# Optimization experiments

Hardware: AMD Instinct MI355X
Metric: run time of the kernel (lower is better)

The kernel has to match this reference:

```python
import jax, jax.numpy as jnp
import numpy as np
from jax.scipy.special import logsumexp

_INF = 1e8
_GAMMA_MIN = 1e-4


def _cosine_cost(x, y):
    # 1 - cosine similarity, batched: [B,M,D] x [B,N,D] -> [B,M,N]
    xn = x / jnp.clip(jnp.linalg.norm(x, axis=-1, keepdims=True), 1e-8)
    yn = y / jnp.clip(jnp.linalg.norm(y, axis=-1, keepdims=True), 1e-8)
    return 1.0 - jnp.einsum('bmd,bnd->bmn', xn, yn)


def _soft_dtw_alignment(cost, gv):
    B, M, N = cost.shape
    dt = cost.dtype
    ii = jnp.arange(M)          # full diagonal index range, masked per step

    # ---- forward DP: R[b, i+1, j+1] = C[i,j] + softmin(R[i,j], R[i,j+1], R[i+1,j]) ----
    R0 = jnp.full((B, M + 1, N + 1), _INF, dtype=dt).at[:, 0, 0].set(0.0)

    def fstep(R, d):
        jj = d - ii
        valid = (jj >= 0) & (jj < N)            # (M,)
        jjc = jnp.clip(jj, 0, N - 1)
        ip, jp = ii + 1, jjc + 1
        p = jnp.stack([R[:, ip - 1, jp - 1],
                       R[:, ip - 1, jp],
                       R[:, ip, jp - 1]], axis=-1)          # (B, M, 3)
        soft = -gv * logsumexp(p / -gv, axis=-1)            # soft-min
        new = cost[:, ii, jjc] + soft                       # (B, M)
        cur = R[:, ip, jp]
        R = R.at[:, ip, jp].set(jnp.where(valid[None, :], new, cur))
        return R, None

    R, _ = jax.lax.scan(fstep, R0, jnp.arange(M + N - 1))
    distance = R[:, M, N]

    # ---- backward DP for alignment matrix E ----
    E0 = jnp.zeros((B, M + 2, N + 2), dtype=dt).at[:, M, N].set(1.0)
    Re = jnp.full((B, M + 2, N + 2), -_INF, dtype=dt).at[:, :M + 1, :N + 1].set(R)
    Ce = jnp.zeros((B, M + 2, N + 2), dtype=dt).at[:, 1:M + 1, 1:N + 1].set(cost)

    def bstep(E, d):
        jj = d - ii
        valid = (jj >= 0) & (jj < N)
        jjc = jnp.clip(jj, 0, N - 1)
        ip, jp = ii + 1, jjc + 1
        rc = Re[:, ip, jp]
        wd = jnp.exp(jnp.clip((Re[:, ip + 1, jp + 1] - Ce[:, ip + 1, jp + 1] - rc) / gv, -50, 50))
        wn = jnp.exp(jnp.clip((Re[:, ip + 1, jp] - Ce[:, ip + 1, jp] - rc) / gv, -50, 50))
        wr = jnp.exp(jnp.clip((Re[:, ip, jp + 1] - Ce[:, ip, jp + 1] - rc) / gv, -50, 50))
        new = E[:, ip + 1, jp + 1] * wd + E[:, ip + 1, jp] * wn + E[:, ip, jp + 1] * wr
        cur = E[:, ip, jp]
        E = E.at[:, ip, jp].set(jnp.where(valid[None, :], new, cur))
        return E, None

    E, _ = jax.lax.scan(bstep, E0, jnp.arange(M + N - 3, -1, -1))
    alignment = E[:, 1:M + 1, 1:N + 1]
    return alignment, distance


def setup_inputs() -> dict:
    key = jax.random.key(0)
    k1, k2 = jax.random.split(key)
    B, M, N, D = 8, 256, 256, 512
    x = jax.random.normal(k1, (B, M, D), dtype=jnp.float32)
    y = jax.random.normal(k2, (B, N, D), dtype=jnp.float32)
    gamma = jnp.asarray(1.0, dtype=jnp.float32)   # learned nn.Parameter
    return {"x": x, "y": y, "gamma": gamma}


def reference(x, y, gamma):
    cost = _cosine_cost(x, y)
    gv = jnp.maximum(jnp.abs(gamma), _GAMMA_MIN)   # effective gamma
    alignment, distance = _soft_dtw_alignment(cost, gv)
    return alignment, distance
```

## Files before the change

### kernel.cpp

```cpp
#include <hip/hip_runtime.h>

#define USTR 192

#define EXP2F(x) __builtin_amdgcn_exp2f(x)
#define LOG2F(x) __builtin_amdgcn_logf(x)

__device__ __forceinline__ void ld4(float d[4], const float* p) {
  float4 v = *(const float4*)p;
  d[0] = v.x; d[1] = v.y; d[2] = v.z; d[3] = v.w;
}

__global__ void __launch_bounds__(256) norms_kernel(const float* __restrict__ x,
                                                    const float* __restrict__ y,
                                                    float* __restrict__ rnx,
                                                    float* __restrict__ rny) {
  int g = blockIdx.x * 4 + (threadIdx.x >> 6);
  int lane = threadIdx.x & 63;
  const float* src; float* dst; int row;
  if (g < 2048) { src = x; dst = rnx; row = g; }
  else          { src = y; dst = rny; row = g - 2048; }
  const float* p = src + (size_t)row * 512;
  float4 v0 = *(const float4*)(p + lane * 4);
  float4 v1 = *(const float4*)(p + 256 + lane * 4);
  float s = v0.x*v0.x + v0.y*v0.y + v0.z*v0.z + v0.w*v0.w
          + v1.x*v1.x + v1.y*v1.y + v1.z*v1.z + v1.w*v1.w;
#pragma unroll
  for (int o = 32; o > 0; o >>= 1) s += __shfl_xor(s, o, 64);
  if (lane == 0) dst[row] = 1.0f / fmaxf(sqrtf(s), 1e-8f);
}

__global__ void __launch_bounds__(256) cost_gemm(const float* __restrict__ x,
                                                 const float* __restrict__ y,
                                                 const float* __restrict__ rnx,
                                                 const float* __restrict__ rny,
                                                 const float* __restrict__ gamma,
                                                 float* __restrict__ mAll) {
  int b = blockIdx.z, mt = blockIdx.y, nt = blockIdx.x;
  int m0 = mt * 32, n0 = nt * 64;
  __shared__ float Xs[16][36];
  __shared__ float Ys[16][68];
  int tid = threadIdx.x;
  int row = tid >> 2, cq = tid & 3;
  int tx = tid & 15, ty = tid >> 4;
  const float* xb = x + ((size_t)b * 256 + m0) * 512;
  const float* yb = y + ((size_t)b * 256 + n0) * 512;
  float acc[2][4] = {};
  for (int k0 = 0; k0 < 512; k0 += 16) {
    float4 xv;
    if (tid < 128) xv = *(const float4*)(xb + (size_t)row * 512 + k0 + cq * 4);
    float4 yv = *(const float4*)(yb + (size_t)row * 512 + k0 + cq * 4);
    __syncthreads();
    if (tid < 128) {
      Xs[cq*4+0][row] = xv.x; Xs[cq*4+1][row] = xv.y;
      Xs[cq*4+2][row] = xv.z; Xs[cq*4+3][row] = xv.w;
    }
    Ys[cq*4+0][row] = yv.x; Ys[cq*4+1][row] = yv.y;
    Ys[cq*4+2][row] = yv.z; Ys[cq*4+3][row] = yv.w;
    __syncthreads();
#pragma unroll
    for (int kk = 0; kk < 16; ++kk) {
      float a0 = Xs[kk][ty * 2 + 0];
      float a1 = Xs[kk][ty * 2 + 1];
      float4 bv = *(const float4*)(&Ys[kk][tx * 4]);
      float br[4] = {bv.x, bv.y, bv.z, bv.w};
#pragma unroll
      for (int c = 0; c < 4; ++c) {
        acc[0][c] += a0 * br[c];
        acc[1][c] += a1 * br[c];
      }
    }
  }
  float gv = fmaxf(fabsf(gamma[0]), 1e-4f);
  float ig2 = 1.4426950408889634f / gv;
  float rx[2], ry[4];
#pragma unroll
  for (int r = 0; r < 2; ++r) rx[r] = rnx[b * 256 + m0 + ty * 2 + r];
#pragma unroll
  for (int c = 0; c < 4; ++c) ry[c] = rny[b * 256 + n0 + tx * 4 + c];
  int l = nt * 16 + tx;
  int v = mt * 16 + ty;
  int u = v + l;
  float4 stm[2];
#pragma unroll
  for (int r = 0; r < 2; ++r) {
    float c0 = (1.0f - acc[r][0] * rx[r] * ry[0]) * ig2;
    float c1 = (1.0f - acc[r][1] * rx[r] * ry[1]) * ig2;
    float c2 = (1.0f - acc[r][2] * rx[r] * ry[2]) * ig2;
    float c3 = (1.0f - acc[r][3] * rx[r] * ry[3]) * ig2;
    stm[r] = (float4){EXP2F(-c0), EXP2F(-c1), EXP2F(-c2), EXP2F(-c3)};
  }
  float* mpF = mAll + ((size_t)b * USTR + u) * 512 + l * 8;
  *(float4*)(mpF)     = stm[0];
  *(float4*)(mpF + 4) = stm[1];
  float* mpR = mAll + ((size_t)(8 + b) * USTR + (190 - u)) * 512 + (63 - l) * 8;
  *(float4*)(mpR)     = (float4){stm[1].w, stm[1].z, stm[1].y, stm[1].x};
  *(float4*)(mpR + 4) = (float4){stm[0].w, stm[0].z, stm[0].y, stm[0].x};
}

__global__ void __launch_bounds__(64, 1) pass_kernel(const float* __restrict__ mAll,
                                                     float* __restrict__ pAll,
                                                     float* __restrict__ QepAll,
                                                     const float* __restrict__ gamma,
                                                     float* __restrict__ dist_out) {
  int blk = blockIdx.x, l = threadIdx.x;
  int dir = blk >> 3, b = blk & 7;
  float gv = fmaxf(fabsf(gamma[0]), 1e-4f);
  float gl = gv * 0.6931471805599453f;
  const float* mb = mAll + (size_t)blk * USTR * 512 + l * 8;
  float* pb = pAll + (size_t)blk * USTR * 512 + l * 8;
  float* qe = QepAll + ((size_t)blk * 64 + l) * 24;
  float Pp0 = 0.f, Pp1 = 0.f, Pp2 = 0.f, Pp3 = 0.f;
  float bot0 = 0.f, bot1 = 0.f;
  int Q = 0;
  float ucar = (l == 0) ? 1.0f : 0.f;
  float A0[8], A1[8], A2[8], A3[8], A4[8], A5[8], A6[8], A7[8];
  float A8[8], A9[8], A10[8], A11[8], A12[8], A13[8], A14[8], A15[8];
  auto loadC = [&](int t, float* buf) {
    int u = t > 190 ? 190 : t;
    const float* p = mb + (size_t)u * 512;
    ld4(buf, p); ld4(buf + 4, p + 4);
  };
  auto body = [&](int t, const float* mm) {
    bool act = (unsigned)(t - l) <= 127u;
    float s0 = __shfl_up(bot0, 1);
    float s1 = __shfl_up(bot1, 1);
    int  liQ = __shfl_up(Q, 1);
    if (l == 0) { s0 = 0.f; s1 = 0.f; }
    else { int adj = liQ - Q; s0 = ldexpf(s0, adj); s1 = ldexpf(s1, adj); }
    float v0 = mm[0] * (Pp0 + s0 + ucar);
    float v1 = mm[1] * (Pp1 + v0 + Pp0);
    float v2 = mm[2] * (Pp2 + v1 + Pp1);
    float v3 = mm[3] * (Pp3 + v2 + Pp2);
    float w0 = mm[4] * (v0 + s1 + s0);
    float w1 = mm[5] * (v1 + w0 + v0);
    float w2 = mm[6] * (v2 + w1 + v1);
    float w3 = mm[7] * (v3 + w2 + v2);
    if (act) {
      float* sp = pb + (size_t)t * 512;
      *(float4*)(sp)     = (float4){v0, v1, v2, v3};
      *(float4*)(sp + 4) = (float4){w0, w1, w2, w3};
      Pp0 = w0; Pp1 = w1; Pp2 = w2; Pp3 = w3;
      ucar = s1; bot0 = v3; bot1 = w3;
      if (dir == 0 && l == 63 && t == 190)
        dist_out[b] = (-(float)Q - LOG2F(w3)) * gl;
    }
  };
  auto renorm = [&](int tEnd) {
    if ((unsigned)(tEnd - l) <= 127u) {
      int e = (int)((__float_as_uint(Pp3) >> 23) & 255u) - 127;
      Pp0 = ldexpf(Pp0, -e); Pp1 = ldexpf(Pp1, -e);
      Pp2 = ldexpf(Pp2, -e); Pp3 = ldexpf(Pp3, -e);
      ucar = ldexpf(ucar, -e);
      bot0 = ldexpf(bot0, -e); bot1 = ldexpf(bot1, -e);
      Q += e;
    }
  };
  loadC(0, A0);  loadC(1, A1);  loadC(2, A2);  loadC(3, A3);
  loadC(4, A4);  loadC(5, A5);  loadC(6, A6);  loadC(7, A7);
  loadC(8, A8);  loadC(9, A9);  loadC(10, A10); loadC(11, A11);
  loadC(12, A12); loadC(13, A13); loadC(14, A14); loadC(15, A15);
  for (int it = 0; it < 12; ++it) {
    int s = it * 16;
    qe[2 * it] = (float)Q;
    body(s + 0, A0); loadC(s + 16, A0);
    body(s + 1, A1); loadC(s + 17, A1);
    body(s + 2, A2); loadC(s + 18, A2);
    body(s + 3, A3); loadC(s + 19, A3);
    body(s + 4, A4); loadC(s + 20, A4);
    body(s + 5, A5); loadC(s + 21, A5);
    body(s + 6, A6); loadC(s + 22, A6);
    body(s + 7, A7); loadC(s + 23, A7);
    renorm(s + 7);
    qe[2 * it + 1] = (float)Q;
    body(s + 8,  A8);  loadC(s + 24, A8);
    body(s + 9,  A9);  loadC(s + 25, A9);
    body(s + 10, A10); loadC(s + 26, A10);
    body(s + 11, A11); loadC(s + 27, A11);
    body(s + 12, A12); loadC(s + 28, A12);
    body(s + 13, A13); loadC(s + 29, A13);
    body(s + 14, A14); loadC(s + 30, A14);
    body(s + 15, A15); loadC(s + 31, A15);
    renorm(s + 15);
  }
}

__global__ void __launch_bounds__(256) e_kernel(const float* __restrict__ mAll,
                                                const float* __restrict__ pAll,
                                                const float* __restrict__ QepAll,
                                                float* __restrict__ out) {
  int tid = blockIdx.x * 256 + threadIdx.x;
  int l = tid & 63;
  int r = (tid >> 6) & 255;
  int b = tid >> 14;
  int v = r >> 1, rf = r & 1;
  int uF = v + l;
  int uR = 190 - v - l;
  const float* pF  = pAll + ((size_t)b * USTR + uF) * 512 + l * 8 + rf * 4;
  const float* pRv = pAll + ((size_t)(8 + b) * USTR + uR) * 512 + (63 - l) * 8 + (1 - rf) * 4;
  const float* mF  = mAll + ((size_t)b * USTR + uF) * 512 + l * 8 + rf * 4;
  float P[4], Bv[4], M[4];
  ld4(P, pF); ld4(Bv, pRv); ld4(M, mF);
  float Qf = QepAll[((size_t)b * 64 + l) * 24 + (uF >> 3)];
  float Qb = QepAll[((size_t)(8 + b) * 64 + (63 - l)) * 24 + (uR >> 3)];
  float Zp = pAll[((size_t)b * USTR + 190) * 512 + 511];
  float Zq = QepAll[((size_t)b * 64 + 63) * 24 + 23];
  int e = (int)(Qf + Qb - Zq);
  float inv = 1.0f / Zp;
  float4 o;
  o.x = ldexpf(P[0] * Bv[3] / M[0] * inv, e);
  o.y = ldexpf(P[1] * Bv[2] / M[1] * inv, e);
  o.z = ldexpf(P[2] * Bv[1] / M[2] * inv, e);
  o.w = ldexpf(P[3] * Bv[0] / M[3] * inv, e);
  *(float4*)(out + (size_t)b * 65536 + (size_t)r * 256 + 4 * l) = o;
}

extern "C" void kernel_launch(void* const* d_in, const int* in_sizes, int n_in,
                              void* d_out, int out_size, void* d_ws, size_t ws_size,
                              hipStream_t stream) {
  const float* x = (const float*)d_in[0];
  const float* y = (const float*)d_in[1];
  const float* gamma = (const float*)d_in[2];
  float* out = (float*)d_out;
  float* ws = (float*)d_ws;

  const size_t PMAT = (size_t)16 * USTR * 512;
  float* rnx    = ws;
  float* rny    = ws + 2048;
  float* mAll   = ws + 4096;
  float* pAll   = mAll + PMAT;
  float* QepAll = pAll + PMAT;

  norms_kernel<<<1024, 256, 0, stream>>>(x, y, rnx, rny);
  cost_gemm<<<dim3(4, 8, 8), 256, 0, stream>>>(x, y, rnx, rny, gamma, mAll);
  pass_kernel<<<16, 64, 0, stream>>>(mAll, pAll, QepAll, gamma, out + 524288);
  e_kernel<<<512, 256, 0, stream>>>(mAll, pAll, QepAll, out);
}
```

Measured before the change: 125.7 us.

## Fuse row-norm computation into cost GEMM and double-buffer its K tiles

Removes the separate norms kernel: row sums of squares are accumulated from the tiles already loaded by the cost GEMM, reduced with lane shuffles, and kept in shared memory. The GEMM main loop now uses K tiles of 32 with double-buffered shared memory and prefetches the next tile into registers during compute, halving the barriers per K. This saves one launch and a re-read of x and y, at the cost of more registers and shared memory per block.

```diff
diff --git a/kernel.cpp b/kernel.cpp
--- a/kernel.cpp
+++ b/kernel.cpp
@@ -10,58 +10,61 @@
   d[0] = v.x; d[1] = v.y; d[2] = v.z; d[3] = v.w;
 }
 
-__global__ void __launch_bounds__(256) norms_kernel(const float* __restrict__ x,
-                                                    const float* __restrict__ y,
-                                                    float* __restrict__ rnx,
-                                                    float* __restrict__ rny) {
-  int g = blockIdx.x * 4 + (threadIdx.x >> 6);
-  int lane = threadIdx.x & 63;
-  const float* src; float* dst; int row;
-  if (g < 2048) { src = x; dst = rnx; row = g; }
-  else          { src = y; dst = rny; row = g - 2048; }
-  const float* p = src + (size_t)row * 512;
-  float4 v0 = *(const float4*)(p + lane * 4);
-  float4 v1 = *(const float4*)(p + 256 + lane * 4);
-  float s = v0.x*v0.x + v0.y*v0.y + v0.z*v0.z + v0.w*v0.w
-          + v1.x*v1.x + v1.y*v1.y + v1.z*v1.z + v1.w*v1.w;
-#pragma unroll
-  for (int o = 32; o > 0; o >>= 1) s += __shfl_xor(s, o, 64);
-  if (lane == 0) dst[row] = 1.0f / fmaxf(sqrtf(s), 1e-8f);
-}
-
 __global__ void __launch_bounds__(256) cost_gemm(const float* __restrict__ x,
                                                  const float* __restrict__ y,
-                                                 const float* __restrict__ rnx,
-                                                 const float* __restrict__ rny,
                                                  const float* __restrict__ gamma,
                                                  float* __restrict__ mAll) {
   int b = blockIdx.z, mt = blockIdx.y, nt = blockIdx.x;
   int m0 = mt * 32, n0 = nt * 64;
-  __shared__ float Xs[16][36];
-  __shared__ float Ys[16][68];
+  __shared__ float Xs[2][32][36];
+  __shared__ float Ys[2][32][68];
+  __shared__ float RxS[32];
+  __shared__ float RyS[64];
   int tid = threadIdx.x;
   int row = tid >> 2, cq = tid & 3;
   int tx = tid & 15, ty = tid >> 4;
   const float* xb = x + ((size_t)b * 256 + m0) * 512;
   const float* yb = y + ((size_t)b * 256 + n0) * 512;
   float acc[2][4] = {};
-  for (int k0 = 0; k0 < 512; k0 += 16) {
-    float4 xv;
-    if (tid < 128) xv = *(const float4*)(xb + (size_t)row * 512 + k0 + cq * 4);
-    float4 yv = *(const float4*)(yb + (size_t)row * 512 + k0 + cq * 4);
+  float sx = 0.f, sy = 0.f;
+  float4 xv0, xv1, yv0, yv1;
+
+  auto loadTile = [&](int k0) {
+    if (tid < 128) {
+      xv0 = *(const float4*)(xb + (size_t)row * 512 + k0 + cq * 4);
+      xv1 = *(const float4*)(xb + (size_t)row * 512 + k0 + 16 + cq * 4);
+    }
+    yv0 = *(const float4*)(yb + (size_t)row * 512 + k0 + cq * 4);
+    yv1 = *(const float4*)(yb + (size_t)row * 512 + k0 + 16 + cq * 4);
+  };
+  auto stageTile = [&](int buf) {
+    if (tid < 128) {
+      sx += xv0.x*xv0.x + xv0.y*xv0.y + xv0.z*xv0.z + xv0.w*xv0.w
+          + xv1.x*xv1.x + xv1.y*xv1.y + xv1.z*xv1.z + xv1.w*xv1.w;
+      Xs[buf][cq*4+0][row] = xv0.x; Xs[buf][cq*4+1][row] = xv0.y;
+      Xs[buf][cq*4+2][row] = xv0.z; Xs[buf][cq*4+3][row] = xv0.w;
+      Xs[buf][16+cq*4+0][row] = xv1.x; Xs[buf][16+cq*4+1][row] = xv1.y;
+      Xs[buf][16+cq*4+2][row] = xv1.z; Xs[buf][16+cq*4+3][row] = xv1.w;
+    }
+    sy += yv0.x*yv0.x + yv0.y*yv0.y + yv0.z*yv0.z + yv0.w*yv0.w
+        + yv1.x*yv1.x + yv1.y*yv1.y + yv1.z*yv1.z + yv1.w*yv1.w;
+    Ys[buf][cq*4+0][row] = yv0.x; Ys[buf][cq*4+1][row] = yv0.y;
+    Ys[buf][cq*4+2][row] = yv0.z; Ys[buf][cq*4+3][row] = yv0.w;
+    Ys[buf][16+cq*4+0][row] = yv1.x; Ys[buf][16+cq*4+1][row] = yv1.y;
+    Ys[buf][16+cq*4+2][row] = yv1.z; Ys[buf][16+cq*4+3][row] = yv1.w;
+  };
+
+  loadTile(0);
+  stageTile(0);
+  for (int t = 0; t < 16; ++t) {
     __syncthreads();
-    if (tid < 128) {
-      Xs[cq*4+0][row] = xv.x; Xs[cq*4+1][row] = xv.y;
-      Xs[cq*4+2][row] = xv.z; Xs[cq*4+3][row] = xv.w;
-    }
-    Ys[cq*4+0][row] = yv.x; Ys[cq*4+1][row] = yv.y;
-    Ys[cq*4+2][row] = yv.z; Ys[cq*4+3][row] = yv.w;
-    __syncthreads();
-#pragma unroll
-    for (int kk = 0; kk < 16; ++kk) {
-      float a0 = Xs[kk][ty * 2 + 0];
-      float a1 = Xs[kk][ty * 2 + 1];
-      float4 bv = *(const float4*)(&Ys[kk][tx * 4]);
+    if (t < 15) loadTile((t + 1) * 32);
+    int cb = t & 1;
+#pragma unroll
+    for (int kk = 0; kk < 32; ++kk) {
+      float a0 = Xs[cb][kk][ty * 2 + 0];
+      float a1 = Xs[cb][kk][ty * 2 + 1];
+      float4 bv = *(const float4*)(&Ys[cb][kk][tx * 4]);
       float br[4] = {bv.x, bv.y, bv.z, bv.w};
 #pragma unroll
       for (int c = 0; c < 4; ++c) {
@@ -69,14 +72,24 @@
         acc[1][c] += a1 * br[c];
       }
     }
-  }
+    if (t < 15) stageTile(cb ^ 1);
+  }
+
+  sy += __shfl_xor(sy, 1, 64); sy += __shfl_xor(sy, 2, 64);
+  if (tid < 128) { sx += __shfl_xor(sx, 1, 64); sx += __shfl_xor(sx, 2, 64); }
+  if (cq == 0) {
+    RyS[row] = 1.0f / fmaxf(sqrtf(sy), 1e-8f);
+    if (tid < 128) RxS[row] = 1.0f / fmaxf(sqrtf(sx), 1e-8f);
+  }
+  __syncthreads();
+
   float gv = fmaxf(fabsf(gamma[0]), 1e-4f);
   float ig2 = 1.4426950408889634f / gv;
   float rx[2], ry[4];
 #pragma unroll
-  for (int r = 0; r < 2; ++r) rx[r] = rnx[b * 256 + m0 + ty * 2 + r];
-#pragma unroll
-  for (int c = 0; c < 4; ++c) ry[c] = rny[b * 256 + n0 + tx * 4 + c];
+  for (int r = 0; r < 2; ++r) rx[r] = RxS[ty * 2 + r];
+#pragma unroll
+  for (int c = 0; c < 4; ++c) ry[c] = RyS[tx * 4 + c];
   int l = nt * 16 + tx;
   int v = mt * 16 + ty;
   int u = v + l;
@@ -224,14 +237,11 @@
   float* ws = (float*)d_ws;
 
   const size_t PMAT = (size_t)16 * USTR * 512;
-  float* rnx    = ws;
-  float* rny    = ws + 2048;
   float* mAll   = ws + 4096;
   float* pAll   = mAll + PMAT;
   float* QepAll = pAll + PMAT;
 
-  norms_kernel<<<1024, 256, 0, stream>>>(x, y, rnx, rny);
-  cost_gemm<<<dim3(4, 8, 8), 256, 0, stream>>>(x, y, rnx, rny, gamma, mAll);
+  cost_gemm<<<dim3(4, 8, 8), 256, 0, stream>>>(x, y, gamma, mAll);
   pass_kernel<<<16, 64, 0, stream>>>(mAll, pAll, QepAll, gamma, out + 524288);
   e_kernel<<<512, 256, 0, stream>>>(mAll, pAll, QepAll, out);
 }
```

Result: faster. 116.3 us (-7.5%).
